# Kernel optimization log

Measured on AMD Instinct MI355X. Metric: run time of the kernel, lower is better.

The kernel has to match this reference:

```python
import jax, jax.numpy as jnp
import numpy as np

N_NODES = 10000
N_EDGES = 160000
F_IN, D, N_CLS = 300, 1024, 10
NEG_SLOPE = 0.2


def setup_inputs() -> dict:
    key = jax.random.key(0)
    ks = jax.random.split(key, 12)
    s = 0.05  # small init scale for numerical sanity
    return {
        "x": jax.random.normal(ks[0], (N_NODES, F_IN), jnp.float32),
        "edge_index": jax.random.randint(ks[1], (2, N_EDGES), 0, N_NODES, jnp.int64),
        "W1": jax.random.normal(ks[2], (F_IN, D), jnp.float32) * s,
        "att_src1": jax.random.normal(ks[3], (D,), jnp.float32) * s,
        "att_dst1": jax.random.normal(ks[4], (D,), jnp.float32) * s,
        "b1": jnp.zeros((D,), jnp.float32),
        "W2": jax.random.normal(ks[5], (D, D), jnp.float32) * s,
        "att_src2": jax.random.normal(ks[6], (D,), jnp.float32) * s,
        "att_dst2": jax.random.normal(ks[7], (D,), jnp.float32) * s,
        "b2": jnp.zeros((D,), jnp.float32),
        "fc_w": jax.random.normal(ks[8], (D, N_CLS), jnp.float32) * s,
        "fc_b": jnp.zeros((N_CLS,), jnp.float32),
    }


def gat_conv(x, src, dst, W, a_src, a_dst, b):
    # PyG GATConv, heads=1: h = x W; e_ij = leaky_relu(a_src.h_j + a_dst.h_i)
    h = x @ W                      # [N, D]
    e = jax.nn.leaky_relu((h @ a_src)[src] + (h @ a_dst)[dst], NEG_SLOPE)  # [E]
    # scatter-softmax over edges grouped by destination node
    m = jax.lax.stop_gradient(jax.ops.segment_max(e, dst, num_segments=N_NODES))
    ex = jnp.exp(e - m[dst])
    denom = jax.ops.segment_sum(ex, dst, num_segments=N_NODES)
    alpha = ex / denom[dst]        # [E]
    out = jax.ops.segment_sum(alpha[:, None] * h[src], dst, num_segments=N_NODES)
    return out + b


def reference(x, edge_index, W1, att_src1, att_dst1, b1,
              W2, att_src2, att_dst2, b2, fc_w, fc_b):
    loops = jnp.arange(N_NODES, dtype=edge_index.dtype)
    src = jnp.concatenate([edge_index[0], loops])  # add_self_loops=True
    dst = jnp.concatenate([edge_index[1], loops])
    emb = jax.nn.relu(gat_conv(x, src, dst, W1, att_src1, att_dst1, b1))
    emb = jax.nn.relu(gat_conv(emb, src, dst, W2, att_src2, att_dst2, b2))
    return jax.nn.softmax(emb @ fc_w + fc_b, axis=-1)
```

## Files before the change

kernel.cpp:

```cpp
#include <hip/hip_runtime.h>
#include <hip/hip_bf16.h>
#include <hip/hip_fp16.h>
#include <math.h>

#define N_NODES 10000
#define N_EDGES 160000
#define E_TOT   (N_EDGES + N_NODES)
#define F_IN    300
#define D       1024
#define N_CLS   10
#define NEG_SLOPE 0.2f

#define MP      10112
#define KP1     320
#define KP2     1024

typedef __attribute__((ext_vector_type(8))) _Float16 f16x8;
typedef __attribute__((ext_vector_type(4))) float f32x4;

#define GLOAD_LDS16(g, l) __builtin_amdgcn_global_load_lds( \
    (const __attribute__((address_space(1))) void*)(g), \
    (__attribute__((address_space(3))) void*)(l), 16, 0, 0)


__global__ void count_edges(const int* __restrict__ dst, int* __restrict__ deg) {
    int e = blockIdx.x * blockDim.x + threadIdx.x;
    if (e < N_EDGES) atomicAdd(&deg[dst[e]], 1);
}

__global__ void scan_offs(const int* __restrict__ deg, int* __restrict__ offs,
                          int* __restrict__ pos) {
    __shared__ int sbuf[1024];
    __shared__ int scarry;
    int t = threadIdx.x;
    if (t == 0) { scarry = 0; offs[0] = 0; }
    __syncthreads();
    for (int base = 0; base < N_NODES; base += 1024) {
        int v = (base + t < N_NODES) ? deg[base + t] : 0;
        sbuf[t] = v;
        __syncthreads();
        for (int off = 1; off < 1024; off <<= 1) {
            int add = (t >= off) ? sbuf[t - off] : 0;
            __syncthreads();
            sbuf[t] += add;
            __syncthreads();
        }
        int carry = scarry;
        if (base + t < N_NODES) {
            int incl = carry + sbuf[t];
            offs[base + t + 1] = incl;
            pos[base + t]      = incl - v;
        }
        __syncthreads();
        if (t == 1023) scarry = carry + sbuf[1023];
        __syncthreads();
    }
}

__global__ void scatter_edges(const int* __restrict__ src, const int* __restrict__ dst,
                              int* __restrict__ pos, int* __restrict__ ssrc) {
    int e = blockIdx.x * blockDim.x + threadIdx.x;
    if (e < N_EDGES) {
        int d = dst[e];
        int p = atomicAdd(&pos[d], 1);
        ssrc[p] = src[e];
    } else if (e < E_TOT) {
        int i = e - N_EDGES;
        int p = atomicAdd(&pos[i], 1);
        ssrc[p] = i;
    }
}


#define ZR1 (112 * KP1)
#define ZR2 (N_NODES * 20)
#define ZR3 (112 * KP2)
#define ZTOT (2*ZR1 + 2*ZR2 + 2*ZR3 + 2*N_NODES)

#define ZONE_A 331
#define ZONE_B 320
#define ZONE_C 1024
#define ZONE_D ((ZTOT + N_NODES + 255) / 256)

__global__ __launch_bounds__(256) void mega_prep(
        const float* __restrict__ W1, const float* __restrict__ as1,
        const float* __restrict__ ad1, const float* __restrict__ W2,
        const float* __restrict__ as2, const float* __restrict__ ad2,
        float* __restrict__ u1, float* __restrict__ v1,
        float* __restrict__ u2, float* __restrict__ v2,
        _Float16* __restrict__ BT1h, _Float16* __restrict__ BT2h,
        float* __restrict__ hs2, float* __restrict__ hd2,
        unsigned short* __restrict__ Ah1, unsigned short* __restrict__ Al1,
        unsigned short* __restrict__ Ah2, unsigned short* __restrict__ Al2,
        int* __restrict__ deg) {
    __shared__ float tile[32][33];
    int b = blockIdx.x;
    int t = threadIdx.x;

    if (b < ZONE_A) {
        int wid  = (b * 256 + t) >> 6;
        int lane = t & 63;
        const float* row; const float* a; const float* bb; float *du, *dv; int k;
        if (wid < F_IN) {
            k = wid; row = W1 + (size_t)k * D; a = as1; bb = ad1; du = u1; dv = v1;
        } else {
            k = wid - F_IN; row = W2 + (size_t)k * D; a = as2; bb = ad2; du = u2; dv = v2;
        }
        float s1 = 0.f, s2 = 0.f;
        for (int n = lane; n < D; n += 64) {
            float w = row[n];
            s1 += w * a[n];
            s2 += w * bb[n];
        }
        #pragma unroll
        for (int o = 32; o; o >>= 1) { s1 += __shfl_xor(s1, o); s2 += __shfl_xor(s2, o); }
        if (lane == 0) { du[k] = s1; dv[k] = s2; }
        return;
    }
    if (b < ZONE_A + ZONE_B + ZONE_C) {
        const float* W; _Float16* BT; int K, Kp, b2;
        if (b < ZONE_A + ZONE_B) { b2 = b - ZONE_A; W = W1; BT = BT1h; K = F_IN; Kp = KP1;
            int kb = b2 % (KP1 / 32), nb = b2 / (KP1 / 32);
            int k0 = kb * 32, n0 = nb * 32;
            int tx = t & 31, ty = t >> 5;
            #pragma unroll
            for (int j = 0; j < 32; j += 8) {
                int k = k0 + ty + j;
                tile[ty + j][tx] = (k < K) ? W[(size_t)k * D + n0 + tx] : 0.f;
            }
            __syncthreads();
            #pragma unroll
            for (int j = 0; j < 32; j += 8)
                BT[(size_t)(n0 + ty + j) * Kp + k0 + tx] = (_Float16)tile[tx][ty + j];
        } else { b2 = b - ZONE_A - ZONE_B; W = W2; BT = BT2h; K = D; Kp = KP2;
            int kb = b2 & 31, nb = b2 >> 5;
            int k0 = kb * 32, n0 = nb * 32;
            int tx = t & 31, ty = t >> 5;
            #pragma unroll
            for (int j = 0; j < 32; j += 8) {
                int k = k0 + ty + j;
                tile[ty + j][tx] = (k < K) ? W[(size_t)k * D + n0 + tx] : 0.f;
            }
            __syncthreads();
            #pragma unroll
            for (int j = 0; j < 32; j += 8)
                BT[(size_t)(n0 + ty + j) * Kp + k0 + tx] = (_Float16)tile[tx][ty + j];
        }
        return;
    }
    int idx = (b - ZONE_A - ZONE_B - ZONE_C) * 256 + t;
    if (idx >= ZTOT + N_NODES) return;
    if (idx >= ZTOT) { deg[idx - ZTOT] = 1; return; }
    if (idx < 2 * ZR1) {
        unsigned short* B = (idx < ZR1) ? Ah1 : Al1;
        int off = (idx < ZR1) ? idx : idx - ZR1;
        B[(size_t)N_NODES * KP1 + off] = 0;
    } else if ((idx -= 2 * ZR1) < 2 * ZR2) {
        unsigned short* B = (idx < ZR2) ? Ah1 : Al1;
        int off = (idx < ZR2) ? idx : idx - ZR2;
        int r = off / 20, c = 300 + off % 20;
        B[(size_t)r * KP1 + c] = 0;
    } else if ((idx -= 2 * ZR2) < 2 * ZR3) {
        unsigned short* B = (idx < ZR3) ? Ah2 : Al2;
        int off = (idx < ZR3) ? idx : idx - ZR3;
        B[(size_t)N_NODES * KP2 + off] = 0;
    } else {
        idx -= 2 * ZR3;
        if (idx < N_NODES) hs2[idx] = 0.f;
        else hd2[idx - N_NODES] = 0.f;
    }
}


__global__ void node_scores_x(const float* __restrict__ x, const float* __restrict__ u1,
                              const float* __restrict__ v1, float* __restrict__ hs,
                              float* __restrict__ hd) {
    int wid  = (int)((blockIdx.x * blockDim.x + threadIdx.x) >> 6);
    int lane = threadIdx.x & 63;
    if (wid >= N_NODES) return;
    const float* row = x + (size_t)wid * F_IN;
    float s1 = 0.f, s2 = 0.f;
    for (int k = lane; k < F_IN; k += 64) {
        float v = row[k];
        s1 += v * u1[k];
        s2 += v * v1[k];
    }
    #pragma unroll
    for (int o = 32; o; o >>= 1) { s1 += __shfl_xor(s1, o); s2 += __shfl_xor(s2, o); }
    if (lane == 0) { hs[wid] = s1; hd[wid] = s2; }
}


__global__ __launch_bounds__(256) void aggregate_x(
        const float* __restrict__ x, const float* __restrict__ hs,
        const float* __restrict__ hd, const int* __restrict__ offs,
        const int* __restrict__ ssrc, _Float16* __restrict__ outh,
        _Float16* __restrict__ outl) {
    int i = blockIdx.x;
    int t = threadIdx.x;
    int lane = t & 63;
    int wv = t >> 6;
    int start = offs[i], end = offs[i + 1];
    __shared__ float red[8];
    __shared__ float part[2][75][4];
    float hdi = hd[i];

    float lmax = -INFINITY;
    for (int p = start + t; p < end; p += 256) {
        float s = hs[ssrc[p]] + hdi;
        s = (s >= 0.f) ? s : s * NEG_SLOPE;
        lmax = fmaxf(lmax, s);
    }
    #pragma unroll
    for (int o = 32; o; o >>= 1) lmax = fmaxf(lmax, __shfl_xor(lmax, o));
    if (lane == 0) red[wv] = lmax;
    __syncthreads();
    float m = fmaxf(fmaxf(red[0], red[1]), fmaxf(red[2], red[3]));

    float lsum = 0.f;
    for (int p = start + t; p < end; p += 256) {
        float s = hs[ssrc[p]] + hdi;
        s = (s >= 0.f) ? s : s * NEG_SLOPE;
        lsum += __expf(s - m);
    }
    #pragma unroll
    for (int o = 32; o; o >>= 1) lsum += __shfl_xor(lsum, o);
    if (lane == 0) red[4 + wv] = lsum;
    __syncthreads();
    float inv = 1.0f / (red[4] + red[5] + red[6] + red[7]);

    int g = t / 75;
    int s = t - g * 75;
    int c = s * 4;
    float4 a = {0.f, 0.f, 0.f, 0.f};
    if (t < 225) {
        int p = start + g;
        for (; p + 3 < end; p += 6) {
            int j0 = ssrc[p], j1 = ssrc[p + 3];
            float s0 = hs[j0] + hdi; s0 = (s0 >= 0.f) ? s0 : s0 * NEG_SLOPE;
            float s1 = hs[j1] + hdi; s1 = (s1 >= 0.f) ? s1 : s1 * NEG_SLOPE;
            float w0 = __expf(s0 - m), w1 = __expf(s1 - m);
            float4 v0 = *(const float4*)(x + (size_t)j0 * F_IN + c);
            float4 v1 = *(const float4*)(x + (size_t)j1 * F_IN + c);
            a.x += w0 * v0.x + w1 * v1.x;
            a.y += w0 * v0.y + w1 * v1.y;
            a.z += w0 * v0.z + w1 * v1.z;
            a.w += w0 * v0.w + w1 * v1.w;
        }
        if (p < end) {
            int j0 = ssrc[p];
            float s0 = hs[j0] + hdi; s0 = (s0 >= 0.f) ? s0 : s0 * NEG_SLOPE;
            float w0 = __expf(s0 - m);
            float4 v0 = *(const float4*)(x + (size_t)j0 * F_IN + c);
            a.x += w0 * v0.x; a.y += w0 * v0.y; a.z += w0 * v0.z; a.w += w0 * v0.w;
        }
    }
    if (t < 225 && g > 0) {
        part[g - 1][s][0] = a.x; part[g - 1][s][1] = a.y;
        part[g - 1][s][2] = a.z; part[g - 1][s][3] = a.w;
    }
    __syncthreads();
    if (t < 75) {
        a.x += part[0][t][0] + part[1][t][0];
        a.y += part[0][t][1] + part[1][t][1];
        a.z += part[0][t][2] + part[1][t][2];
        a.w += part[0][t][3] + part[1][t][3];
        float rv[4] = {a.x * inv, a.y * inv, a.z * inv, a.w * inv};
        _Float16 hi4[4], lo4[4];
        #pragma unroll
        for (int q = 0; q < 4; ++q) {
            _Float16 hi = (_Float16)rv[q];
            hi4[q] = hi;
            lo4[q] = (_Float16)(rv[q] - (float)hi);
        }
        *(float2*)(outh + (size_t)i * KP1 + c) = *(float2*)hi4;
        *(float2*)(outl + (size_t)i * KP1 + c) = *(float2*)lo4;
    }
}


__global__ __launch_bounds__(256) void aggregate_d(
        const _Float16* __restrict__ h, const float* __restrict__ hs,
        const float* __restrict__ hd, const int* __restrict__ offs,
        const int* __restrict__ ssrc, _Float16* __restrict__ outh,
        _Float16* __restrict__ outl) {
    int i = blockIdx.x;
    int t = threadIdx.x;
    int lane = t & 63;
    int wv = t >> 6;
    int start = offs[i], end = offs[i + 1];
    __shared__ float red[8];
    __shared__ float part[128][8];
    float hdi = hd[i];

    float lmax = -INFINITY;
    for (int p = start + t; p < end; p += 256) {
        float s = hs[ssrc[p]] + hdi;
        s = (s >= 0.f) ? s : s * NEG_SLOPE;
        lmax = fmaxf(lmax, s);
    }
    #pragma unroll
    for (int o = 32; o; o >>= 1) lmax = fmaxf(lmax, __shfl_xor(lmax, o));
    if (lane == 0) red[wv] = lmax;
    __syncthreads();
    float m = fmaxf(fmaxf(red[0], red[1]), fmaxf(red[2], red[3]));

    float lsum = 0.f;
    for (int p = start + t; p < end; p += 256) {
        float s = hs[ssrc[p]] + hdi;
        s = (s >= 0.f) ? s : s * NEG_SLOPE;
        lsum += __expf(s - m);
    }
    #pragma unroll
    for (int o = 32; o; o >>= 1) lsum += __shfl_xor(lsum, o);
    if (lane == 0) red[4 + wv] = lsum;
    __syncthreads();
    float inv = 1.0f / (red[4] + red[5] + red[6] + red[7]);

    int g = t >> 7;
    int s = t & 127;
    int c = s * 8;
    float a0[8] = {}, a1[8] = {}, a2[8] = {}, a3[8] = {};
    int p = start + g;
    for (; p + 6 < end; p += 8) {
        int j0 = ssrc[p], j1 = ssrc[p + 2], j2 = ssrc[p + 4], j3 = ssrc[p + 6];
        float s0 = hs[j0] + hdi; s0 = (s0 >= 0.f) ? s0 : s0 * NEG_SLOPE;
        float s1 = hs[j1] + hdi; s1 = (s1 >= 0.f) ? s1 : s1 * NEG_SLOPE;
        float s2 = hs[j2] + hdi; s2 = (s2 >= 0.f) ? s2 : s2 * NEG_SLOPE;
        float s3 = hs[j3] + hdi; s3 = (s3 >= 0.f) ? s3 : s3 * NEG_SLOPE;
        float w0 = __expf(s0 - m), w1 = __expf(s1 - m);
        float w2 = __expf(s2 - m), w3 = __expf(s3 - m);
        f16x8 v0 = *(const f16x8*)(h + (size_t)j0 * D + c);
        f16x8 v1 = *(const f16x8*)(h + (size_t)j1 * D + c);
        f16x8 v2 = *(const f16x8*)(h + (size_t)j2 * D + c);
        f16x8 v3 = *(const f16x8*)(h + (size_t)j3 * D + c);
        #pragma unroll
        for (int q = 0; q < 8; ++q) {
            a0[q] += w0 * (float)v0[q];
            a1[q] += w1 * (float)v1[q];
            a2[q] += w2 * (float)v2[q];
            a3[q] += w3 * (float)v3[q];
        }
    }
    for (; p < end; p += 2) {
        int j0 = ssrc[p];
        float s0 = hs[j0] + hdi; s0 = (s0 >= 0.f) ? s0 : s0 * NEG_SLOPE;
        float w0 = __expf(s0 - m);
        f16x8 v0 = *(const f16x8*)(h + (size_t)j0 * D + c);
        #pragma unroll
        for (int q = 0; q < 8; ++q) a0[q] += w0 * (float)v0[q];
    }
    float af[8];
    #pragma unroll
    for (int q = 0; q < 8; ++q) af[q] = (a0[q] + a1[q]) + (a2[q] + a3[q]);
    if (g == 1) {
        #pragma unroll
        for (int q = 0; q < 8; ++q) part[s][q] = af[q];
    }
    __syncthreads();
    if (t < 128) {
        _Float16 hi8[8], lo8[8];
        #pragma unroll
        for (int q = 0; q < 8; ++q) {
            float rv = (af[q] + part[t][q]) * inv;
            _Float16 hi = (_Float16)rv;
            hi8[q] = hi;
            lo8[q] = (_Float16)(rv - (float)hi);
        }
        *(float4*)(outh + (size_t)i * KP2 + c) = *(float4*)hi8;
        *(float4*)(outl + (size_t)i * KP2 + c) = *(float4*)lo8;
    }
}


__global__ __launch_bounds__(256) void gemm_split_mfma(
        const _Float16* __restrict__ Ah, const _Float16* __restrict__ Al,
        const _Float16* __restrict__ BTh,
        float* __restrict__ Cf, _Float16* __restrict__ Ch,
        const float* __restrict__ bias,
        const float* __restrict__ asrc, const float* __restrict__ adst,
        float* __restrict__ hs, float* __restrict__ hd,
        int Mreal, int Kp, int dots) {
    __shared__ char lds[49152];
    const int t    = threadIdx.x;
    const int lane = t & 63;
    const int wid  = t >> 6;
    const int chunkg = (int)gridDim.x >> 3;
    const int vid  = ((int)blockIdx.x & 7) * chunkg + ((int)blockIdx.x >> 3);
    const int n0 = (vid & 7) * 128;
    const int m0 = (vid >> 3) * 128;
    const int wr = (wid >> 1) * 64;
    const int wc = (wid & 1) * 64;
    const int fr = lane & 15;
    const int kg = lane >> 4;

    const int r0 = t >> 2, s0 = t & 3;
    const int r1 = r0 + 64;
    const int g0 = (s0 ^ ((r0 >> 1) & 3)) << 3;
    const int g1 = (s0 ^ ((r1 >> 1) & 3)) << 3;
    const size_t oA0 = (size_t)(m0 + r0) * Kp + g0;
    const size_t oA1 = (size_t)(m0 + r1) * Kp + g1;
    const size_t oB0 = (size_t)(n0 + r0) * Kp + g0;
    const size_t oB1 = (size_t)(n0 + r1) * Kp + g1;
    const int ko = (kg ^ ((fr >> 1) & 3)) << 4;

    f32x4 acc[4][4] = {};

    auto STAGE = [&](int b, int kb) {
        char* base = lds + b * 24576;
        GLOAD_LDS16(Ah  + oA0 + kb, base + t * 16);
        GLOAD_LDS16(Ah  + oA1 + kb, base + 4096  + t * 16);
        GLOAD_LDS16(Al  + oA0 + kb, base + 8192  + t * 16);
        GLOAD_LDS16(Al  + oA1 + kb, base + 12288 + t * 16);
        GLOAD_LDS16(BTh + oB0 + kb, base + 16384 + t * 16);
        GLOAD_LDS16(BTh + oB1 + kb, base + 20480 + t * 16);
    };

    STAGE(0, 0);
    __syncthreads();

    int cur = 0;
    for (int kb = 0; kb < Kp; kb += 32) {
        if (kb + 32 < Kp) STAGE(cur ^ 1, kb + 32);
        char* base = lds + cur * 24576;
        f16x8 ah[4], al[4], bh[4];
        #pragma unroll
        for (int f = 0; f < 4; ++f) {
            int ra = (wr + f * 16 + fr) * 64 + ko;
            int rb = (wc + f * 16 + fr) * 64 + ko;
            ah[f] = *(const f16x8*)(base + ra);
            al[f] = *(const f16x8*)(base + 8192 + ra);
            bh[f] = *(const f16x8*)(base + 16384 + rb);
        }
        #pragma unroll
        for (int fm = 0; fm < 4; ++fm)
            #pragma unroll
            for (int fn = 0; fn < 4; ++fn)
                acc[fm][fn] = __builtin_amdgcn_mfma_f32_16x16x32_f16(
                    ah[fm], bh[fn], acc[fm][fn], 0, 0, 0);
        #pragma unroll
        for (int fm = 0; fm < 4; ++fm)
            #pragma unroll
            for (int fn = 0; fn < 4; ++fn)
                acc[fm][fn] = __builtin_amdgcn_mfma_f32_16x16x32_f16(
                    al[fm], bh[fn], acc[fm][fn], 0, 0, 0);
        __syncthreads();
        cur ^= 1;
    }

    float bv[4];
    #pragma unroll
    for (int fn = 0; fn < 4; ++fn) bv[fn] = bias[n0 + wc + fn * 16 + fr];
    #pragma unroll
    for (int fm = 0; fm < 4; ++fm) {
        int mb = m0 + wr + fm * 16 + kg * 4;
        #pragma unroll
        for (int fn = 0; fn < 4; ++fn) {
            int cn = n0 + wc + fn * 16 + fr;
            #pragma unroll
            for (int j = 0; j < 4; ++j) {
                float r = fmaxf(acc[fm][fn][j] + bv[fn], 0.f);
                acc[fm][fn][j] = r;
                int m = mb + j;
                if (m < Mreal) {
                    if (Cf) Cf[(size_t)m * 1024 + cn] = r;
                    else    Ch[(size_t)m * 1024 + cn] = (_Float16)r;
                }
            }
        }
    }

    if (dots) {
        float av[4], dv[4];
        #pragma unroll
        for (int fn = 0; fn < 4; ++fn) {
            int cn = n0 + wc + fn * 16 + fr;
            av[fn] = asrc[cn];
            dv[fn] = adst[cn];
        }
        #pragma unroll
        for (int fm = 0; fm < 4; ++fm) {
            #pragma unroll
            for (int j = 0; j < 4; ++j) {
                float v1 = acc[fm][0][j] * av[0] + acc[fm][1][j] * av[1]
                         + acc[fm][2][j] * av[2] + acc[fm][3][j] * av[3];
                float v2 = acc[fm][0][j] * dv[0] + acc[fm][1][j] * dv[1]
                         + acc[fm][2][j] * dv[2] + acc[fm][3][j] * dv[3];
                #pragma unroll
                for (int o = 1; o < 16; o <<= 1) {
                    v1 += __shfl_xor(v1, o);
                    v2 += __shfl_xor(v2, o);
                }
                int m = m0 + wr + fm * 16 + kg * 4 + j;
                if (fr == 0 && m < Mreal) {
                    atomicAdd(&hs[m], v1);
                    atomicAdd(&hd[m], v2);
                }
            }
        }
    }
}


__global__ void fc_softmax(const _Float16* __restrict__ emb, const float* __restrict__ fcw,
                           const float* __restrict__ fcb, float* __restrict__ out) {
    int wid  = (int)((blockIdx.x * blockDim.x + threadIdx.x) >> 6);
    int lane = threadIdx.x & 63;
    if (wid >= N_NODES) return;
    float acc[N_CLS] = {};
    const _Float16* row = emb + (size_t)wid * D;
    for (int k = lane * 8; k < D; k += 512) {
        f16x8 v = *(const f16x8*)(row + k);
        #pragma unroll
        for (int q = 0; q < 8; ++q) {
            float vv = (float)v[q];
            #pragma unroll
            for (int c = 0; c < N_CLS; ++c) acc[c] += vv * fcw[(k + q) * N_CLS + c];
        }
    }
    #pragma unroll
    for (int c = 0; c < N_CLS; ++c) {
        #pragma unroll
        for (int o = 32; o; o >>= 1) acc[c] += __shfl_xor(acc[c], o);
    }
    if (lane == 0) {
        float logit[N_CLS];
        float m = -INFINITY;
        #pragma unroll
        for (int c = 0; c < N_CLS; ++c) { logit[c] = acc[c] + fcb[c]; m = fmaxf(m, logit[c]); }
        float s = 0.f;
        #pragma unroll
        for (int c = 0; c < N_CLS; ++c) { logit[c] = __expf(logit[c] - m); s += logit[c]; }
        float invs = 1.0f / s;
        #pragma unroll
        for (int c = 0; c < N_CLS; ++c) out[(size_t)wid * N_CLS + c] = logit[c] * invs;
    }
}


extern "C" void kernel_launch(void* const* d_in, const int* in_sizes, int n_in,
                              void* d_out, int out_size, void* d_ws, size_t ws_size,
                              hipStream_t stream) {
    const float* x        = (const float*)d_in[0];
    const int*   ei       = (const int*)d_in[1];
    const float* W1       = (const float*)d_in[2];
    const float* att_src1 = (const float*)d_in[3];
    const float* att_dst1 = (const float*)d_in[4];
    const float* b1       = (const float*)d_in[5];
    const float* W2       = (const float*)d_in[6];
    const float* att_src2 = (const float*)d_in[7];
    const float* att_dst2 = (const float*)d_in[8];
    const float* b2       = (const float*)d_in[9];
    const float* fc_w     = (const float*)d_in[10];
    const float* fc_b     = (const float*)d_in[11];
    float* out = (float*)d_out;

    const int* src = ei;
    const int* dst = ei + N_EDGES;

    char* w = (char*)d_ws;
    #define ALLOC(name, bytes) char* name = w; w += (((size_t)(bytes) + 255) & ~(size_t)255)
    ALLOC(p_emb1h, (size_t)N_NODES * D * 2);
    ALLOC(p_emb2h, (size_t)N_NODES * D * 2);
    ALLOC(p_hs1,   (size_t)N_NODES * 4);
    ALLOC(p_hd1,   (size_t)N_NODES * 4);
    ALLOC(p_hs2,   (size_t)N_NODES * 4);
    ALLOC(p_hd2,   (size_t)N_NODES * 4);
    ALLOC(p_deg,   (size_t)N_NODES * 4);
    ALLOC(p_offs,  (size_t)(N_NODES + 1) * 4);
    ALLOC(p_pos,   (size_t)N_NODES * 4);
    ALLOC(p_ssrc,  (size_t)E_TOT * 4);
    ALLOC(p_u1,    (size_t)F_IN * 4);
    ALLOC(p_v1,    (size_t)F_IN * 4);
    ALLOC(p_u2,    (size_t)D * 4);
    ALLOC(p_v2,    (size_t)D * 4);
    ALLOC(p_as1,   (size_t)2 * MP * KP1 * 2);
    ALLOC(p_as2,   (size_t)2 * MP * KP2 * 2);
    ALLOC(p_bt1,   (size_t)D * KP1 * 2);
    ALLOC(p_bt2,   (size_t)D * KP2 * 2);
    #undef ALLOC

    _Float16* emb1h = (_Float16*)p_emb1h;
    _Float16* emb2h = (_Float16*)p_emb2h;
    float* hs1  = (float*)p_hs1;
    float* hd1  = (float*)p_hd1;
    float* hs2  = (float*)p_hs2;
    float* hd2  = (float*)p_hd2;
    int*   deg  = (int*)p_deg;
    int*   offs = (int*)p_offs;
    int*   pos  = (int*)p_pos;
    int*   ssrc = (int*)p_ssrc;
    float* u1 = (float*)p_u1; float* v1 = (float*)p_v1;
    float* u2 = (float*)p_u2; float* v2 = (float*)p_v2;
    _Float16* Ah1  = (_Float16*)p_as1;
    _Float16* Al1  = Ah1 + (size_t)MP * KP1;
    _Float16* Ah2  = (_Float16*)p_as2;
    _Float16* Al2  = Ah2 + (size_t)MP * KP2;
    _Float16* BT1h = (_Float16*)p_bt1;
    _Float16* BT2h = (_Float16*)p_bt2;

    mega_prep<<<ZONE_A + ZONE_B + ZONE_C + ZONE_D, 256, 0, stream>>>(
        W1, att_src1, att_dst1, W2, att_src2, att_dst2,
        u1, v1, u2, v2, BT1h, BT2h, hs2, hd2,
        (unsigned short*)Ah1, (unsigned short*)Al1,
        (unsigned short*)Ah2, (unsigned short*)Al2, deg);

    count_edges<<<(N_EDGES + 255) / 256, 256, 0, stream>>>(dst, deg);
    scan_offs<<<1, 1024, 0, stream>>>(deg, offs, pos);
    scatter_edges<<<(E_TOT + 255) / 256, 256, 0, stream>>>(src, dst, pos, ssrc);

    const int gemmGrid = (D / 128) * (MP / 128);

    node_scores_x<<<(N_NODES * 64 + 255) / 256, 256, 0, stream>>>(x, u1, v1, hs1, hd1);
    aggregate_x<<<N_NODES, 256, 0, stream>>>(x, hs1, hd1, offs, ssrc, Ah1, Al1);
    gemm_split_mfma<<<gemmGrid, 256, 0, stream>>>(Ah1, Al1, BT1h,
                                                  (float*)nullptr, emb1h, b1,
                                                  u2, v2, hs2, hd2, N_NODES, KP1, 1);

    aggregate_d<<<N_NODES, 256, 0, stream>>>(emb1h, hs2, hd2, offs, ssrc, Ah2, Al2);
    gemm_split_mfma<<<gemmGrid, 256, 0, stream>>>(Ah2, Al2, BT2h,
                                                  (float*)nullptr, emb2h, b2,
                                                  (const float*)nullptr, (const float*)nullptr,
                                                  (float*)nullptr, (float*)nullptr,
                                                  N_NODES, KP2, 0);

    fc_softmax<<<(N_NODES * 64 + 255) / 256, 256, 0, stream>>>(emb2h, fc_w, fc_b, out);
}
```

Baseline: 332.3 us.

## Triple-buffer GEMM LDS staging with vmcnt waits; cache softmax weights in LDS

The split-fp16 MFMA GEMM moves from double to triple buffering. Two stages are now prefetched ahead, and explicit s_waitcnt vmcnt levels plus raw barriers replace the blanket __syncthreads, so global->LDS loads overlap more compute. The aggregation kernels store the per-edge exp weights in an LDS cache during the sum pass and reuse them in the gather pass instead of recomputing hs gathers and exps, falling back when degree exceeds 1024. Partial-sum LDS arrays are padded against bank conflicts, and the weight-transpose code is specialized per matrix. The extra LDS from the third buffer lowers possible occupancy, and the hand-tuned vmcnt counts depend on the exact number of loads issued per stage.

```diff
diff --git a/kernel.cpp b/kernel.cpp
--- a/kernel.cpp
+++ b/kernel.cpp
@@ -14,6 +14,7 @@
 #define MP      10112
 #define KP1     320
 #define KP2     1024
+#define WCAP    1024
 
 typedef __attribute__((ext_vector_type(8))) _Float16 f16x8;
 typedef __attribute__((ext_vector_type(4))) float f32x4;
@@ -118,33 +119,34 @@
         return;
     }
     if (b < ZONE_A + ZONE_B + ZONE_C) {
-        const float* W; _Float16* BT; int K, Kp, b2;
-        if (b < ZONE_A + ZONE_B) { b2 = b - ZONE_A; W = W1; BT = BT1h; K = F_IN; Kp = KP1;
+        if (b < ZONE_A + ZONE_B) {
+            int b2 = b - ZONE_A;
             int kb = b2 % (KP1 / 32), nb = b2 / (KP1 / 32);
             int k0 = kb * 32, n0 = nb * 32;
             int tx = t & 31, ty = t >> 5;
             #pragma unroll
             for (int j = 0; j < 32; j += 8) {
                 int k = k0 + ty + j;
-                tile[ty + j][tx] = (k < K) ? W[(size_t)k * D + n0 + tx] : 0.f;
+                tile[ty + j][tx] = (k < F_IN) ? W1[(size_t)k * D + n0 + tx] : 0.f;
             }
             __syncthreads();
             #pragma unroll
             for (int j = 0; j < 32; j += 8)
-                BT[(size_t)(n0 + ty + j) * Kp + k0 + tx] = (_Float16)tile[tx][ty + j];
-        } else { b2 = b - ZONE_A - ZONE_B; W = W2; BT = BT2h; K = D; Kp = KP2;
+                BT1h[(size_t)(n0 + ty + j) * KP1 + k0 + tx] = (_Float16)tile[tx][ty + j];
+        } else {
+            int b2 = b - ZONE_A - ZONE_B;
             int kb = b2 & 31, nb = b2 >> 5;
             int k0 = kb * 32, n0 = nb * 32;
             int tx = t & 31, ty = t >> 5;
             #pragma unroll
             for (int j = 0; j < 32; j += 8) {
                 int k = k0 + ty + j;
-                tile[ty + j][tx] = (k < K) ? W[(size_t)k * D + n0 + tx] : 0.f;
+                tile[ty + j][tx] = W2[(size_t)k * D + n0 + tx];
             }
             __syncthreads();
             #pragma unroll
             for (int j = 0; j < 32; j += 8)
-                BT[(size_t)(n0 + ty + j) * Kp + k0 + tx] = (_Float16)tile[tx][ty + j];
+                BT2h[(size_t)(n0 + ty + j) * KP2 + k0 + tx] = (_Float16)tile[tx][ty + j];
         }
         return;
     }
@@ -202,7 +204,8 @@
     int wv = t >> 6;
     int start = offs[i], end = offs[i + 1];
     __shared__ float red[8];
-    __shared__ float part[2][75][4];
+    __shared__ float part[2][75][5];
+    __shared__ float wcache[WCAP];
     float hdi = hd[i];
 
     float lmax = -INFINITY;
@@ -221,13 +224,17 @@
     for (int p = start + t; p < end; p += 256) {
         float s = hs[ssrc[p]] + hdi;
         s = (s >= 0.f) ? s : s * NEG_SLOPE;
-        lsum += __expf(s - m);
+        float ex = __expf(s - m);
+        int q = p - start;
+        if (q < WCAP) wcache[q] = ex;
+        lsum += ex;
     }
     #pragma unroll
     for (int o = 32; o; o >>= 1) lsum += __shfl_xor(lsum, o);
     if (lane == 0) red[4 + wv] = lsum;
     __syncthreads();
     float inv = 1.0f / (red[4] + red[5] + red[6] + red[7]);
+    bool cached = (end - start) <= WCAP;
 
     int g = t / 75;
     int s = t - g * 75;
@@ -237,9 +244,13 @@
         int p = start + g;
         for (; p + 3 < end; p += 6) {
             int j0 = ssrc[p], j1 = ssrc[p + 3];
-            float s0 = hs[j0] + hdi; s0 = (s0 >= 0.f) ? s0 : s0 * NEG_SLOPE;
-            float s1 = hs[j1] + hdi; s1 = (s1 >= 0.f) ? s1 : s1 * NEG_SLOPE;
-            float w0 = __expf(s0 - m), w1 = __expf(s1 - m);
+            float w0, w1;
+            if (cached) { w0 = wcache[p - start]; w1 = wcache[p + 3 - start]; }
+            else {
+                float s0 = hs[j0] + hdi; s0 = (s0 >= 0.f) ? s0 : s0 * NEG_SLOPE;
+                float s1 = hs[j1] + hdi; s1 = (s1 >= 0.f) ? s1 : s1 * NEG_SLOPE;
+                w0 = __expf(s0 - m); w1 = __expf(s1 - m);
+            }
             float4 v0 = *(const float4*)(x + (size_t)j0 * F_IN + c);
             float4 v1 = *(const float4*)(x + (size_t)j1 * F_IN + c);
             a.x += w0 * v0.x + w1 * v1.x;
@@ -249,8 +260,12 @@
         }
         if (p < end) {
             int j0 = ssrc[p];
-            float s0 = hs[j0] + hdi; s0 = (s0 >= 0.f) ? s0 : s0 * NEG_SLOPE;
-            float w0 = __expf(s0 - m);
+            float w0;
+            if (cached) w0 = wcache[p - start];
+            else {
+                float s0 = hs[j0] + hdi; s0 = (s0 >= 0.f) ? s0 : s0 * NEG_SLOPE;
+                w0 = __expf(s0 - m);
+            }
             float4 v0 = *(const float4*)(x + (size_t)j0 * F_IN + c);
             a.x += w0 * v0.x; a.y += w0 * v0.y; a.z += w0 * v0.z; a.w += w0 * v0.w;
         }
@@ -290,7 +305,8 @@
     int wv = t >> 6;
     int start = offs[i], end = offs[i + 1];
     __shared__ float red[8];
-    __shared__ float part[128][8];
+    __shared__ float part[128][9];
+    __shared__ float wcache[WCAP];
     float hdi = hd[i];
 
     float lmax = -INFINITY;
@@ -309,13 +325,17 @@
     for (int p = start + t; p < end; p += 256) {
         float s = hs[ssrc[p]] + hdi;
         s = (s >= 0.f) ? s : s * NEG_SLOPE;
-        lsum += __expf(s - m);
+        float ex = __expf(s - m);
+        int q = p - start;
+        if (q < WCAP) wcache[q] = ex;
+        lsum += ex;
     }
     #pragma unroll
     for (int o = 32; o; o >>= 1) lsum += __shfl_xor(lsum, o);
     if (lane == 0) red[4 + wv] = lsum;
     __syncthreads();
     float inv = 1.0f / (red[4] + red[5] + red[6] + red[7]);
+    bool cached = (end - start) <= WCAP;
 
     int g = t >> 7;
     int s = t & 127;
@@ -324,12 +344,18 @@
     int p = start + g;
     for (; p + 6 < end; p += 8) {
         int j0 = ssrc[p], j1 = ssrc[p + 2], j2 = ssrc[p + 4], j3 = ssrc[p + 6];
-        float s0 = hs[j0] + hdi; s0 = (s0 >= 0.f) ? s0 : s0 * NEG_SLOPE;
-        float s1 = hs[j1] + hdi; s1 = (s1 >= 0.f) ? s1 : s1 * NEG_SLOPE;
-        float s2 = hs[j2] + hdi; s2 = (s2 >= 0.f) ? s2 : s2 * NEG_SLOPE;
-        float s3 = hs[j3] + hdi; s3 = (s3 >= 0.f) ? s3 : s3 * NEG_SLOPE;
-        float w0 = __expf(s0 - m), w1 = __expf(s1 - m);
-        float w2 = __expf(s2 - m), w3 = __expf(s3 - m);
+        float w0, w1, w2, w3;
+        if (cached) {
+            int q = p - start;
+            w0 = wcache[q]; w1 = wcache[q + 2]; w2 = wcache[q + 4]; w3 = wcache[q + 6];
+        } else {
+            float s0 = hs[j0] + hdi; s0 = (s0 >= 0.f) ? s0 : s0 * NEG_SLOPE;
+            float s1 = hs[j1] + hdi; s1 = (s1 >= 0.f) ? s1 : s1 * NEG_SLOPE;
+            float s2 = hs[j2] + hdi; s2 = (s2 >= 0.f) ? s2 : s2 * NEG_SLOPE;
+            float s3 = hs[j3] + hdi; s3 = (s3 >= 0.f) ? s3 : s3 * NEG_SLOPE;
+            w0 = __expf(s0 - m); w1 = __expf(s1 - m);
+            w2 = __expf(s2 - m); w3 = __expf(s3 - m);
+        }
         f16x8 v0 = *(const f16x8*)(h + (size_t)j0 * D + c);
         f16x8 v1 = *(const f16x8*)(h + (size_t)j1 * D + c);
         f16x8 v2 = *(const f16x8*)(h + (size_t)j2 * D + c);
@@ -344,8 +370,12 @@
     }
     for (; p < end; p += 2) {
         int j0 = ssrc[p];
-        float s0 = hs[j0] + hdi; s0 = (s0 >= 0.f) ? s0 : s0 * NEG_SLOPE;
-        float w0 = __expf(s0 - m);
+        float w0;
+        if (cached) w0 = wcache[p - start];
+        else {
+            float s0 = hs[j0] + hdi; s0 = (s0 >= 0.f) ? s0 : s0 * NEG_SLOPE;
+            w0 = __expf(s0 - m);
+        }
         f16x8 v0 = *(const f16x8*)(h + (size_t)j0 * D + c);
         #pragma unroll
         for (int q = 0; q < 8; ++q) a0[q] += w0 * (float)v0[q];
@@ -381,7 +411,7 @@
         const float* __restrict__ asrc, const float* __restrict__ adst,
         float* __restrict__ hs, float* __restrict__ hd,
         int Mreal, int Kp, int dots) {
-    __shared__ char lds[49152];
+    __shared__ char lds[3 * 24576];
     const int t    = threadIdx.x;
     const int lane = t & 63;
     const int wid  = t >> 6;
@@ -405,6 +435,7 @@
     const int ko = (kg ^ ((fr >> 1) & 3)) << 4;
 
     f32x4 acc[4][4] = {};
+    const int nsteps = Kp >> 5;
 
     auto STAGE = [&](int b, int kb) {
         char* base = lds + b * 24576;
@@ -417,12 +448,17 @@
     };
 
     STAGE(0, 0);
-    __syncthreads();
-
-    int cur = 0;
-    for (int kb = 0; kb < Kp; kb += 32) {
-        if (kb + 32 < Kp) STAGE(cur ^ 1, kb + 32);
-        char* base = lds + cur * 24576;
+    STAGE(1, 32);
+
+    for (int k = 0; k < nsteps; ++k) {
+        if (k + 2 < nsteps) STAGE((k + 2) % 3, (k + 2) << 5);
+        int rem = nsteps - 1 - k;
+        if (rem >= 2)      asm volatile("s_waitcnt vmcnt(12)" ::: "memory");
+        else if (rem == 1) asm volatile("s_waitcnt vmcnt(6)" ::: "memory");
+        else               asm volatile("s_waitcnt vmcnt(0)" ::: "memory");
+        __builtin_amdgcn_s_barrier();
+        __builtin_amdgcn_sched_barrier(0);
+        char* base = lds + (k % 3) * 24576;
         f16x8 ah[4], al[4], bh[4];
         #pragma unroll
         for (int f = 0; f < 4; ++f) {
@@ -444,8 +480,7 @@
             for (int fn = 0; fn < 4; ++fn)
                 acc[fm][fn] = __builtin_amdgcn_mfma_f32_16x16x32_f16(
                     al[fm], bh[fn], acc[fm][fn], 0, 0, 0);
-        __syncthreads();
-        cur ^= 1;
+        __builtin_amdgcn_s_barrier();
     }
 
     float bv[4];
```

New measurement: 342.2 us. 3.0% more time.
